# Performance work log

Measured on AMD Instinct MI355X. Metric: run time of the kernel, lower is better.

The kernel has to match this reference:

```python
import jax, jax.numpy as jnp
import numpy as np

SIZE = 11
SIGMA = 1.5
CHANNELS = 1
C1 = 0.01 ** 2
C2 = 0.03 ** 2


def _gaussian_kernel(size, sigma, channels):
    # 1D gaussian, outer product, normalized; depthwise kernel [C,1,k,k]
    coords = np.arange(size, dtype=np.float32) - (size - 1) / 2.0
    g = np.exp(-(coords ** 2) / (2.0 * sigma ** 2))
    g = g / g.sum()
    k2d = np.outer(g, g).astype(np.float32)
    k = np.tile(k2d[None, None], (channels, 1, 1, 1))  # [C,1,k,k]
    return jnp.asarray(k)


def _depthwise_conv(x, kernel):
    # x: [B,C,H,W], kernel: [C,1,k,k] -> SAME-padded depthwise conv
    pad = SIZE // 2
    return jax.lax.conv_general_dilated(
        x, kernel,
        window_strides=(1, 1),
        padding=[(pad, pad), (pad, pad)],
        dimension_numbers=('NCHW', 'OIHW', 'NCHW'),
        feature_group_count=CHANNELS,
    )


def setup_inputs() -> dict:
    key = jax.random.key(0)
    k1, k2 = jax.random.split(key)
    img_1 = jax.random.uniform(k1, (16, 1, 1024, 1024), dtype=jnp.float32)
    img_2 = jax.random.uniform(k2, (16, 1, 1024, 1024), dtype=jnp.float32)
    kernel = _gaussian_kernel(SIZE, SIGMA, CHANNELS)
    return {"img_1": img_1, "img_2": img_2, "kernel": kernel}


def reference(img_1, img_2, kernel):
    mu_x = _depthwise_conv(img_1, kernel)
    mu_y = _depthwise_conv(img_2, kernel)
    mu_x2 = mu_x * mu_x
    mu_y2 = mu_y * mu_y
    sigma_x2 = _depthwise_conv(img_1 * img_1, kernel) - mu_x2
    sigma_y2 = _depthwise_conv(img_2 * img_2, kernel) - mu_y2
    sigma_xy = _depthwise_conv(img_1 * img_2, kernel) - mu_x * mu_y
    ssim = ((2 * mu_x * mu_y + C1) * (2 * sigma_xy + C2)) / (
        (mu_x2 + mu_y2 + C1) * (sigma_x2 + sigma_y2 + C2))
    return jnp.mean(ssim)
```

## Files before the change

### kernel.cpp

```cpp
#include <hip/hip_runtime.h>

#define H 1024
#define W 1024
#define K 11
#define RAD 5
#define ROWS 64
#define NIN (ROWS + K - 1)
#define BW 256
#define SW 272

typedef float v2f __attribute__((ext_vector_type(2)));

__global__ void zero_out_kernel(float* out) {
    if (threadIdx.x == 0) out[0] = 0.0f;
}

__device__ __forceinline__ v2f pkfma(v2f a, v2f b, v2f c) {
    return __builtin_elementwise_fma(a, b, c);
}

#define SSIM_TAP(P,S) do {                                                    \
    const float w = gw[10 - ((P - S + 11) % 11)];                             \
    const v2f w2v = { w, w };                                                 \
    mu = pkfma(w2v, q##S, mu);                                                \
    sq = pkfma(w2v, t##S, sq);                                                \
    xy = fmaf(w, u##S, xy);                                                   \
} while (0)

#define SSIM_PHASE_LDS2(P) do {                                               \
    const int i = base + (P);                                                 \
    if (i < NIN) {                                                            \
                              \
        float n1m, n2m, n1t = 0.f, n2t = 0.f;                                 \
        {                                                                     \
            int rn = rin0 + i + 2;                                            \
            rn = min(max(rn, 0), H - 1);                                      \
            const float* __restrict__ r1 = p1 + (size_t)rn * W;               \
            const float* __restrict__ r2 = p2 + (size_t)rn * W;               \
            n1m = r1[gmc] * okm;                                              \
            n2m = r2[gmc] * okm;                                              \
            if (tid < 11) { n1t = r1[gtc] * okt; n2t = r2[gtc] * okt; }       \
        }                                                                     \
                                   \
        const float* __restrict__ sA = bufA + (i & 1) * (2 * SW);             \
        const float* __restrict__ sB = sA + SW;                               \
        float x[11], y[11];                                                   \
        _Pragma("unroll")                                                     \
        for (int j = 0; j < 11; ++j) { x[j] = sA[tid + j]; y[j] = sB[tid + j]; } \
                 \
        v2f amx = {0.f,0.f}, amy = {0.f,0.f};                                 \
        v2f axx = {0.f,0.f}, ayy = {0.f,0.f}, axy = {0.f,0.f};                \
        _Pragma("unroll")                                                     \
        for (int e = 0; e < 5; ++e) {                                         \
            v2f w2 = { gw[2*e], gw[2*e+1] };                                  \
            v2f xp = { x[2*e], x[2*e+1] };                                    \
            v2f yp = { y[2*e], y[2*e+1] };                                    \
            v2f wxp = w2 * xp;                                                \
            v2f wyp = w2 * yp;                                                \
            amx += wxp; amy += wyp;                                           \
            axx = pkfma(wxp, xp, axx);                                        \
            ayy = pkfma(wyp, yp, ayy);                                        \
            axy = pkfma(wxp, yp, axy);                                        \
        }                                                                     \
        const float twx = gw[10] * x[10];                                     \
        const float twy = gw[10] * y[10];                                     \
        const float hmx = (amx.x + amx.y) + twx;                              \
        const float hmy = (amy.x + amy.y) + twy;                              \
        const float hxx = fmaf(twx, x[10], axx.x + axx.y);                    \
        const float hyy = fmaf(twy, y[10], ayy.x + ayy.y);                    \
        const float hxy = fmaf(twx, y[10], axy.x + axy.y);                    \
        {                                                                     \
            const int r = rin0 + i;                                           \
            const float sm = ((unsigned)r < (unsigned)H) ? 1.0f : 0.0f;       \
            const v2f sv = { sm, sm };                                        \
            q##P = sv * (v2f){ hmx, hmy };                                    \
            t##P = sv * (v2f){ hxx, hyy };                                    \
            u##P = sm * hxy;                                                  \
        }                                                                     \
                                    \
        if (i >= K - 1) {                                                     \
            v2f mu = {0.f,0.f}, sq = {0.f,0.f}; float xy = 0.f;               \
            SSIM_TAP(P,0); SSIM_TAP(P,1); SSIM_TAP(P,2); SSIM_TAP(P,3);       \
            SSIM_TAP(P,4); SSIM_TAP(P,5); SSIM_TAP(P,6); SSIM_TAP(P,7);       \
            SSIM_TAP(P,8); SSIM_TAP(P,9); SSIM_TAP(P,10);                     \
            const v2f m2 = mu * mu;                                           \
            const float mxy  = mu.x * mu.y;                                   \
            const v2f sg = sq - m2;                                           \
            const float sxyv = xy - mxy;                                      \
            const float num = fmaf(2.0f, mxy,  C1) * fmaf(2.0f, sxyv, C2);    \
            const float den = (m2.x + m2.y + C1) * (sg.x + sg.y + C2);        \
            acc += num * __builtin_amdgcn_rcpf(den);                          \
        }                                                                     \
            \
        float* __restrict__ dA = bufA + ((i + 1) & 1) * (2 * SW);             \
        float* __restrict__ dB = dA + SW;                                     \
        dA[tid] = h1m;                                                        \
        dB[tid] = h2m;                                                        \
        if (tid < 11) { dA[256 + tid] = h1t; dB[256 + tid] = h2t; }           \
        __syncthreads();                                                      \
        h1m = n1m; h2m = n2m; h1t = n1t; h2t = n2t;                           \
    }                                                                         \
} while (0)

__launch_bounds__(256, 3)
__global__ void ssim_kernel(const float* __restrict__ img1,
                            const float* __restrict__ img2,
                            const float* __restrict__ kern,
                            float* __restrict__ out,
                            float inv_n) {
    __shared__ float sbuf[2][2][SW];
    __shared__ float wsum[4];
    float* bufA = &sbuf[0][0][0];

    const int tid = threadIdx.x;
    const int cb  = blockIdx.x * BW;
    const int ry0 = blockIdx.y * ROWS;
    const int b   = blockIdx.z;

    float gw[K];
    #pragma unroll
    for (int t = 0; t < K; ++t) {
        float s = 0.0f;
        #pragma unroll
        for (int j = 0; j < K; ++j) s += kern[t * K + j];
        gw[t] = __int_as_float(__builtin_amdgcn_readfirstlane(__float_as_int(s)));
    }

    const float* __restrict__ p1 = img1 + (size_t)b * H * W;
    const float* __restrict__ p2 = img2 + (size_t)b * H * W;
    const int rin0 = ry0 - RAD;

    const int  gmc_raw = cb - 5 + tid;
    const float okm = ((unsigned)gmc_raw < (unsigned)W) ? 1.0f : 0.0f;
    const int  gmc = min(max(gmc_raw, 0), W - 1);
    const int  gtc_raw = cb + 251 + tid;
    const float okt = ((unsigned)gtc_raw < (unsigned)W) ? 1.0f : 0.0f;
    const int  gtc = min(gtc_raw, W - 1);

    const v2f z2 = {0.f, 0.f};
    v2f q0=z2,q1=z2,q2=z2,q3=z2,q4=z2,q5=z2,q6=z2,q7=z2,q8=z2,q9=z2,q10=z2;
    v2f t0=z2,t1=z2,t2=z2,t3=z2,t4=z2,t5=z2,t6=z2,t7=z2,t8=z2,t9=z2,t10=z2;
    float u0=0,u1=0,u2=0,u3=0,u4=0,u5=0,u6=0,u7=0,u8=0,u9=0,u10=0;
    float acc = 0.0f;
    const float C1 = 1e-4f;
    const float C2 = 9e-4f;

    float h1m, h2m, h1t = 0.f, h2t = 0.f;

    {
        const int r0 = min(max(rin0, 0), H - 1);
        const float* __restrict__ r1 = p1 + (size_t)r0 * W;
        const float* __restrict__ r2 = p2 + (size_t)r0 * W;
        sbuf[0][0][tid] = r1[gmc] * okm;
        sbuf[0][1][tid] = r2[gmc] * okm;
        if (tid < 11) {
            sbuf[0][0][256 + tid] = r1[gtc] * okt;
            sbuf[0][1][256 + tid] = r2[gtc] * okt;
        }
        const int rn = min(max(rin0 + 1, 0), H - 1);
        const float* __restrict__ s1 = p1 + (size_t)rn * W;
        const float* __restrict__ s2 = p2 + (size_t)rn * W;
        h1m = s1[gmc] * okm;
        h2m = s2[gmc] * okm;
        if (tid < 11) { h1t = s1[gtc] * okt; h2t = s2[gtc] * okt; }
        __syncthreads();
    }

    #pragma unroll 1
    for (int it = 0; it < 7; ++it) {
        const int base = it * K;
        SSIM_PHASE_LDS2(0);  SSIM_PHASE_LDS2(1);  SSIM_PHASE_LDS2(2);
        SSIM_PHASE_LDS2(3);  SSIM_PHASE_LDS2(4);  SSIM_PHASE_LDS2(5);
        SSIM_PHASE_LDS2(6);  SSIM_PHASE_LDS2(7);  SSIM_PHASE_LDS2(8);
        SSIM_PHASE_LDS2(9);  SSIM_PHASE_LDS2(10);
    }

    for (int off = 32; off > 0; off >>= 1)
        acc += __shfl_down(acc, off, 64);
    if ((tid & 63) == 0) wsum[tid >> 6] = acc;
    __syncthreads();
    if (tid == 0) {
        const float s = wsum[0] + wsum[1] + wsum[2] + wsum[3];
        atomicAdd(out, s * inv_n);
    }
}

extern "C" void kernel_launch(void* const* d_in, const int* in_sizes, int n_in,
                              void* d_out, int out_size, void* d_ws, size_t ws_size,
                              hipStream_t stream) {
    const float* img1 = (const float*)d_in[0];
    const float* img2 = (const float*)d_in[1];
    const float* kern = (const float*)d_in[2];
    float* out = (float*)d_out;

    const int B = in_sizes[0] / (H * W);
    const float inv_n = 1.0f / ((float)B * (float)H * (float)W);

    zero_out_kernel<<<dim3(1), dim3(64), 0, stream>>>(out);

    dim3 grid(W / BW, H / ROWS, B);
    ssim_kernel<<<grid, dim3(256), 0, stream>>>(img1, img2, kern, out, inv_n);
}
```

Baseline: 195.2 us.

## Give each wavefront a private LDS row buffer and drop block barriers

Each 64-lane wavefront now owns its own double-buffered LDS strip of 64 columns plus a 10-column halo, so the per-row __syncthreads is removed and wavefronts run independently. This targets the barrier stalls paid on every input row. In exchange each wave loads a larger share of redundant halo columns from global memory (10 extra per 64 instead of 10 per 256). Correctness depends on intra-wave lockstep ordering of the LDS writes and reads, since no wave barrier or fence is inserted.

```diff
diff --git a/kernel.cpp b/kernel.cpp
--- a/kernel.cpp
+++ b/kernel.cpp
@@ -7,7 +7,7 @@
 #define ROWS 64
 #define NIN (ROWS + K - 1)
 #define BW 256
-#define SW 272
+#define SWW 80
 
 typedef float v2f __attribute__((ext_vector_type(2)));
 
@@ -27,10 +27,10 @@
     xy = fmaf(w, u##S, xy);                                                   \
 } while (0)
 
-#define SSIM_PHASE_LDS2(P) do {                                               \
+#define SSIM_PHASE_WV(P) do {                                                 \
     const int i = base + (P);                                                 \
     if (i < NIN) {                                                            \
-                              \
+                \
         float n1m, n2m, n1t = 0.f, n2t = 0.f;                                 \
         {                                                                     \
             int rn = rin0 + i + 2;                                            \
@@ -39,14 +39,14 @@
             const float* __restrict__ r2 = p2 + (size_t)rn * W;               \
             n1m = r1[gmc] * okm;                                              \
             n2m = r2[gmc] * okm;                                              \
-            if (tid < 11) { n1t = r1[gtc] * okt; n2t = r2[gtc] * okt; }       \
-        }                                                                     \
-                                   \
-        const float* __restrict__ sA = bufA + (i & 1) * (2 * SW);             \
-        const float* __restrict__ sB = sA + SW;                               \
+            if (lane < 10) { n1t = r1[gtc] * okt; n2t = r2[gtc] * okt; }      \
+        }                                                                     \
+                \
+        const float* __restrict__ sA = wbase + (i & 1) * (2 * SWW);           \
+        const float* __restrict__ sB = sA + SWW;                              \
         float x[11], y[11];                                                   \
         _Pragma("unroll")                                                     \
-        for (int j = 0; j < 11; ++j) { x[j] = sA[tid + j]; y[j] = sB[tid + j]; } \
+        for (int j = 0; j < 11; ++j) { x[j] = sA[lane + j]; y[j] = sB[lane + j]; } \
                  \
         v2f amx = {0.f,0.f}, amy = {0.f,0.f};                                 \
         v2f axx = {0.f,0.f}, ayy = {0.f,0.f}, axy = {0.f,0.f};                \
@@ -92,12 +92,11 @@
             acc += num * __builtin_amdgcn_rcpf(den);                          \
         }                                                                     \
             \
-        float* __restrict__ dA = bufA + ((i + 1) & 1) * (2 * SW);             \
-        float* __restrict__ dB = dA + SW;                                     \
-        dA[tid] = h1m;                                                        \
-        dB[tid] = h2m;                                                        \
-        if (tid < 11) { dA[256 + tid] = h1t; dB[256 + tid] = h2t; }           \
-        __syncthreads();                                                      \
+        float* __restrict__ dA = wbase + ((i + 1) & 1) * (2 * SWW);           \
+        float* __restrict__ dB = dA + SWW;                                    \
+        dA[lane] = h1m;                                                       \
+        dB[lane] = h2m;                                                       \
+        if (lane < 10) { dA[64 + lane] = h1t; dB[64 + lane] = h2t; }          \
         h1m = n1m; h2m = n2m; h1t = n1t; h2t = n2t;                           \
     }                                                                         \
 } while (0)
@@ -108,12 +107,16 @@
                             const float* __restrict__ kern,
                             float* __restrict__ out,
                             float inv_n) {
-    __shared__ float sbuf[2][2][SW];
+    __shared__ float swb[4][2][2][SWW];
     __shared__ float wsum[4];
-    float* bufA = &sbuf[0][0][0];
-
-    const int tid = threadIdx.x;
+
+    const int tid  = threadIdx.x;
+    const int lane = tid & 63;
+    const int wid  = tid >> 6;
+    float* wbase = &swb[wid][0][0][0];
+
     const int cb  = blockIdx.x * BW;
+    const int wc0 = cb + wid * 64;
     const int ry0 = blockIdx.y * ROWS;
     const int b   = blockIdx.z;
 
@@ -130,12 +133,12 @@
     const float* __restrict__ p2 = img2 + (size_t)b * H * W;
     const int rin0 = ry0 - RAD;
 
-    const int  gmc_raw = cb - 5 + tid;
+    const int   gmc_raw = wc0 - 5 + lane;
     const float okm = ((unsigned)gmc_raw < (unsigned)W) ? 1.0f : 0.0f;
-    const int  gmc = min(max(gmc_raw, 0), W - 1);
-    const int  gtc_raw = cb + 251 + tid;
+    const int   gmc = min(max(gmc_raw, 0), W - 1);
+    const int   gtc_raw = wc0 + 59 + lane;
     const float okt = ((unsigned)gtc_raw < (unsigned)W) ? 1.0f : 0.0f;
-    const int  gtc = min(gtc_raw, W - 1);
+    const int   gtc = min(gtc_raw, W - 1);
 
     const v2f z2 = {0.f, 0.f};
     v2f q0=z2,q1=z2,q2=z2,q3=z2,q4=z2,q5=z2,q6=z2,q7=z2,q8=z2,q9=z2,q10=z2;
@@ -151,33 +154,32 @@
         const int r0 = min(max(rin0, 0), H - 1);
         const float* __restrict__ r1 = p1 + (size_t)r0 * W;
         const float* __restrict__ r2 = p2 + (size_t)r0 * W;
-        sbuf[0][0][tid] = r1[gmc] * okm;
-        sbuf[0][1][tid] = r2[gmc] * okm;
-        if (tid < 11) {
-            sbuf[0][0][256 + tid] = r1[gtc] * okt;
-            sbuf[0][1][256 + tid] = r2[gtc] * okt;
+        wbase[lane]        = r1[gmc] * okm;
+        wbase[SWW + lane]  = r2[gmc] * okm;
+        if (lane < 10) {
+            wbase[64 + lane]       = r1[gtc] * okt;
+            wbase[SWW + 64 + lane] = r2[gtc] * okt;
         }
         const int rn = min(max(rin0 + 1, 0), H - 1);
         const float* __restrict__ s1 = p1 + (size_t)rn * W;
         const float* __restrict__ s2 = p2 + (size_t)rn * W;
         h1m = s1[gmc] * okm;
         h2m = s2[gmc] * okm;
-        if (tid < 11) { h1t = s1[gtc] * okt; h2t = s2[gtc] * okt; }
-        __syncthreads();
+        if (lane < 10) { h1t = s1[gtc] * okt; h2t = s2[gtc] * okt; }
     }
 
     #pragma unroll 1
     for (int it = 0; it < 7; ++it) {
         const int base = it * K;
-        SSIM_PHASE_LDS2(0);  SSIM_PHASE_LDS2(1);  SSIM_PHASE_LDS2(2);
-        SSIM_PHASE_LDS2(3);  SSIM_PHASE_LDS2(4);  SSIM_PHASE_LDS2(5);
-        SSIM_PHASE_LDS2(6);  SSIM_PHASE_LDS2(7);  SSIM_PHASE_LDS2(8);
-        SSIM_PHASE_LDS2(9);  SSIM_PHASE_LDS2(10);
+        SSIM_PHASE_WV(0);  SSIM_PHASE_WV(1);  SSIM_PHASE_WV(2);
+        SSIM_PHASE_WV(3);  SSIM_PHASE_WV(4);  SSIM_PHASE_WV(5);
+        SSIM_PHASE_WV(6);  SSIM_PHASE_WV(7);  SSIM_PHASE_WV(8);
+        SSIM_PHASE_WV(9);  SSIM_PHASE_WV(10);
     }
 
     for (int off = 32; off > 0; off >>= 1)
         acc += __shfl_down(acc, off, 64);
-    if ((tid & 63) == 0) wsum[tid >> 6] = acc;
+    if (lane == 0) wsum[wid] = acc;
     __syncthreads();
     if (tid == 0) {
         const float s = wsum[0] + wsum[1] + wsum[2] + wsum[3];
```

Result: no change. 195.4 us (+0.1%).
